# Kernel optimization log

Hardware: AMD Instinct MI355X
Metric: run time of the kernel (lower is better)

## Reference

```python
import jax, jax.numpy as jnp
import numpy as np

N_NODES = 100000
N_EDGES = 1600000
D = 64          # embedding_dim (in_feats == out_feats)
H = 1           # num_heads
NEG_SLOPE = 0.2


def setup_inputs() -> dict:
    key = jax.random.key(0)
    k = jax.random.split(key, 7)
    feat = jax.random.normal(k[0], (N_NODES, D), dtype=jnp.float32)
    W = jax.random.normal(k[1], (D, H * D), dtype=jnp.float32) * (1.0 / np.sqrt(D))
    attn_l = jax.random.normal(k[2], (1, H, D), dtype=jnp.float32) * (1.0 / np.sqrt(D))
    attn_r = jax.random.normal(k[3], (1, H, D), dtype=jnp.float32) * (1.0 / np.sqrt(D))
    bias = jnp.zeros((H * D,), dtype=jnp.float32)
    src = jax.random.randint(k[4], (N_EDGES,), 0, N_NODES, dtype=jnp.int32)
    dst = jax.random.randint(k[5], (N_EDGES,), 0, N_NODES, dtype=jnp.int32)
    return {"feat": feat, "W": W, "attn_l": attn_l, "attn_r": attn_r,
            "bias": bias, "src": src, "dst": dst}


def reference(feat, W, attn_l, attn_r, bias, src, dst):
    # fc (no bias), view to [N, H, D_out]
    ft = (feat @ W).reshape(-1, H, D)                       # [N, H, D]
    # per-node attention halves
    el = jnp.sum(ft * attn_l, axis=-1, keepdims=True)       # [N, H, 1]
    er = jnp.sum(ft * attn_r, axis=-1, keepdims=True)       # [N, H, 1]
    # edge score: u_add_v then leaky_relu
    e = el[src] + er[dst]                                    # [E, H, 1]
    e = jnp.where(e > 0, e, NEG_SLOPE * e)
    # edge softmax over incoming edges of each destination node
    emax = jax.ops.segment_max(e, dst, num_segments=N_NODES)  # [N, H, 1]
    e_exp = jnp.exp(e - emax[dst])
    denom = jax.ops.segment_sum(e_exp, dst, num_segments=N_NODES)  # [N, H, 1]
    a = e_exp / denom[dst]                                   # [E, H, 1]
    # u_mul_e + sum aggregation to destination
    m = ft[src] * a                                          # [E, H, D]
    rst = jax.ops.segment_sum(m, dst, num_segments=N_NODES)  # [N, H, D]
    # residual (Identity since in_feats == out_feats) + bias
    rst = rst + feat.reshape(-1, H, D)
    rst = rst + bias.reshape(1, H, D)
    return rst
```

## Files before the change

kernel.cpp:

```cpp
#include <hip/hip_runtime.h>
#include <hip/hip_fp16.h>
#include <math.h>

#define NN 100000
#define NE 1600000
#define D 64
#define NEG_SLOPE 0.2f
#define BSH 8
#define BMASK 255
#define NBKT 391
#define NB1 196
#define CHUNK 8192
#define BKT_CAP 8192

typedef __attribute__((ext_vector_type(8))) short short8;
typedef __attribute__((ext_vector_type(4))) float f32x4;

template<int CTRL>
__device__ __forceinline__ float dpp_add(float x) {
    int y = __builtin_amdgcn_update_dpp(0, __float_as_int(x), CTRL, 0xf, 0xf, true);
    return x + __int_as_float(y);
}
template<int CTRL>
__device__ __forceinline__ float dpp_max(float x) {
    int xi = __float_as_int(x);
    int y = __builtin_amdgcn_update_dpp(xi, xi, CTRL, 0xf, 0xf, false);
    return fmaxf(x, __int_as_float(y));
}
__device__ __forceinline__ float wave_sum63(float x) {
    x = dpp_add<0x111>(x); x = dpp_add<0x112>(x); x = dpp_add<0x114>(x);
    x = dpp_add<0x118>(x); x = dpp_add<0x142>(x); x = dpp_add<0x143>(x);
    return x;
}
__device__ __forceinline__ float wave_max63(float x) {
    x = dpp_max<0x111>(x); x = dpp_max<0x112>(x); x = dpp_max<0x114>(x);
    x = dpp_max<0x118>(x); x = dpp_max<0x142>(x); x = dpp_max<0x143>(x);
    return x;
}
__device__ __forceinline__ float rdlane_f(float v, int l) {
    return __int_as_float(__builtin_amdgcn_readlane(__float_as_int(v), l));
}
__device__ __forceinline__ unsigned bf16_1(float f) {
    unsigned x = __float_as_uint(f);
    return (x + 0x7fffu + ((x >> 16) & 1u)) >> 16;
}
__device__ __forceinline__ unsigned bfpack(float a, float b) {
    return bf16_1(a) | (bf16_1(b) << 16);
}

__global__ __launch_bounds__(256) void k_bhist(const int* __restrict__ dst,
                                               unsigned* __restrict__ bcnt,
                                               unsigned* __restrict__ blockHist) {
    __shared__ unsigned lh[NBKT];
    int t = threadIdx.x;
    unsigned b0 = blockIdx.x * CHUNK;
    unsigned b1 = min(b0 + CHUNK, (unsigned)NE);
    for (int b = t; b < NBKT; b += 256) lh[b] = 0u;
    __syncthreads();
    const int4* d4 = (const int4*)(dst + b0);
    unsigned n4 = (b1 - b0) >> 2;
    for (unsigned i = t; i < n4; i += 256) {
        int4 v = d4[i];
        atomicAdd(&lh[((unsigned)v.x) >> BSH], 1u);
        atomicAdd(&lh[((unsigned)v.y) >> BSH], 1u);
        atomicAdd(&lh[((unsigned)v.z) >> BSH], 1u);
        atomicAdd(&lh[((unsigned)v.w) >> BSH], 1u);
    }
    __syncthreads();
    unsigned* bh = blockHist + (size_t)blockIdx.x * NBKT;
    for (int b = t; b < NBKT; b += 256) {
        unsigned c = lh[b];
        bh[b] = c;
        if (c) atomicAdd(&bcnt[b], c);
    }
}

__global__ __launch_bounds__(512) void k_bscan(const unsigned* __restrict__ bcnt,
                                               unsigned* __restrict__ bkt_base,
                                               unsigned* __restrict__ bkt_cur) {
    __shared__ unsigned sh[512];
    int t = threadIdx.x;
    sh[t] = (t < NBKT) ? bcnt[t] : 0u;
    __syncthreads();
    for (int off = 1; off < 512; off <<= 1) {
        unsigned u = (t >= off) ? sh[t - off] : 0u;
        __syncthreads();
        sh[t] += u;
        __syncthreads();
    }
    if (t < NBKT) {
        unsigned ex = t ? sh[t - 1] : 0u;
        bkt_base[t] = ex;
        bkt_cur[t] = ex;
    }
}

__global__ __launch_bounds__(256) void k_bin(const int* __restrict__ src,
                                             const int* __restrict__ dst,
                                             unsigned* __restrict__ bkt_cur,
                                             unsigned* __restrict__ binned,
                                             const unsigned* __restrict__ blockHist) {
    __shared__ unsigned lh[NBKT];
    int t = threadIdx.x;
    unsigned b0 = blockIdx.x * CHUNK;
    unsigned b1 = min(b0 + CHUNK, (unsigned)NE);
    const unsigned* bh = blockHist + (size_t)blockIdx.x * NBKT;
    for (int b = t; b < NBKT; b += 256) {
        unsigned c = bh[b];
        lh[b] = c ? atomicAdd(&bkt_cur[b], c) : 0u;
    }
    __syncthreads();
    const int4* d4 = (const int4*)(dst + b0);
    const int4* s4 = (const int4*)(src + b0);
    unsigned n4 = (b1 - b0) >> 2;
    for (unsigned i = t; i < n4; i += 256) {
        int4 dv = d4[i];
        int4 sv = s4[i];
        {   unsigned d_ = (unsigned)dv.x, s_ = (unsigned)sv.x;
            unsigned pos = atomicAdd(&lh[d_ >> BSH], 1u);
            binned[pos] = (s_ << BSH) | (d_ & BMASK); }
        {   unsigned d_ = (unsigned)dv.y, s_ = (unsigned)sv.y;
            unsigned pos = atomicAdd(&lh[d_ >> BSH], 1u);
            binned[pos] = (s_ << BSH) | (d_ & BMASK); }
        {   unsigned d_ = (unsigned)dv.z, s_ = (unsigned)sv.z;
            unsigned pos = atomicAdd(&lh[d_ >> BSH], 1u);
            binned[pos] = (s_ << BSH) | (d_ & BMASK); }
        {   unsigned d_ = (unsigned)dv.w, s_ = (unsigned)sv.w;
            unsigned pos = atomicAdd(&lh[d_ >> BSH], 1u);
            binned[pos] = (s_ << BSH) | (d_ & BMASK); }
    }
}

__global__ __launch_bounds__(256) void k_bsort(const unsigned* __restrict__ bkt_base,
                                               const unsigned* __restrict__ binned,
                                               int* __restrict__ perm,
                                               unsigned* __restrict__ rowp) {
    __shared__ unsigned lh[256];
    __shared__ unsigned cur[256];
    __shared__ unsigned stage[BKT_CAP];
    int t = threadIdx.x;
    int b = blockIdx.x;
    unsigned beg = bkt_base[b];
    unsigned end = (b == NBKT - 1) ? (unsigned)NE : bkt_base[b + 1];
    unsigned cnt = end - beg;
    lh[t] = 0u;
    __syncthreads();
    if (cnt <= BKT_CAP) {
        for (unsigned i = t; i < cnt; i += 256) {
            unsigned w = binned[beg + i];
            stage[i] = w;
            atomicAdd(&lh[w & BMASK], 1u);
        }
    } else {
        for (unsigned i = beg + t; i < end; i += 256)
            atomicAdd(&lh[binned[i] & BMASK], 1u);
    }
    __syncthreads();
    for (int off = 1; off < 256; off <<= 1) {
        unsigned u = (t >= off) ? lh[t - off] : 0u;
        __syncthreads();
        lh[t] += u;
        __syncthreads();
    }
    unsigned start = (t == 0) ? 0u : lh[t - 1];
    unsigned node = ((unsigned)b << BSH) + (unsigned)t;
    if (node <= NN) rowp[node] = beg + start;
    cur[t] = start;
    __syncthreads();
    if (cnt <= BKT_CAP) {
        for (unsigned i = t; i < cnt; i += 256) {
            unsigned w = stage[i];
            unsigned pos = atomicAdd(&cur[w & BMASK], 1u);
            perm[beg + pos] = (int)(w >> BSH);
        }
    } else {
        for (unsigned i = beg + t; i < end; i += 256) {
            unsigned w = binned[i];
            unsigned pos = atomicAdd(&cur[w & BMASK], 1u);
            perm[beg + pos] = (int)(w >> BSH);
        }
    }
}


__global__ __launch_bounds__(256) void k_wprep(const float* __restrict__ W,
                                               const float* __restrict__ attn_l,
                                               const float* __restrict__ attn_r,
                                               float* __restrict__ wl,
                                               float* __restrict__ wr,
                                               unsigned short* __restrict__ Wtb,
                                               unsigned* __restrict__ bcnt) {
    int t = threadIdx.x;
    for (int i = t; i < NBKT; i += 256) bcnt[i] = 0u;
    {   int k = t >> 2, s = t & 3;
        float pl = 0.f, pr = 0.f;
        #pragma unroll
        for (int q = 0; q < 4; ++q) {
            int seg = s + q * 4;
            float4 f = *(const float4*)(W + k * 64 + seg * 4);
            float4 a = *(const float4*)(attn_l + seg * 4);
            float4 b = *(const float4*)(attn_r + seg * 4);
            pl += f.x * a.x + f.y * a.y + f.z * a.z + f.w * a.w;
            pr += f.x * b.x + f.y * b.y + f.z * b.z + f.w * b.w;
        }
        pl += __shfl_xor(pl, 1, 64); pl += __shfl_xor(pl, 2, 64);
        pr += __shfl_xor(pr, 1, 64); pr += __shfl_xor(pr, 2, 64);
        if (s == 0) { wl[k] = pl; wr[k] = pr; }
    }
    {   int j = t & 63, g = t >> 6;
        #pragma unroll
        for (int i = 0; i < 8; ++i) {
            int k0 = g * 16 + i * 2;
            float w0 = W[k0 * 64 + j];
            float w1 = W[(k0 + 1) * 64 + j];
            *(unsigned*)(Wtb + j * 64 + k0) = bfpack(w0, w1);
        }
    }
}

__global__ __launch_bounds__(256) void k1_mfma(const float* __restrict__ feat,
                                               const float* __restrict__ wl,
                                               const float* __restrict__ wr,
                                               const unsigned short* __restrict__ Wtb,
                                               __half* __restrict__ ft,
                                               float* __restrict__ el,
                                               float* __restrict__ er) {
    __shared__ unsigned short Ab[64 * 64];
    __shared__ unsigned short Bb[64 * 64];
    int t = threadIdx.x;
    int n0 = blockIdx.x * 64;

    {
        int j = t >> 2, q = t & 3;
        uint4 w0 = *(const uint4*)(Wtb + j * 64 + q * 16);
        uint4 w1 = *(const uint4*)(Wtb + j * 64 + q * 16 + 8);
        unsigned m = (unsigned)((j & 7) << 4);
        *(uint4*)((char*)Bb + j * 128 + (((unsigned)(q * 32)) ^ m)) = w0;
        *(uint4*)((char*)Bb + j * 128 + (((unsigned)(q * 32 + 16)) ^ m)) = w1;
    }
    {
        int r = t >> 2, s = t & 3;
        int n = n0 + r;
        bool valid = n < NN;
        const float* fp = feat + (size_t)(valid ? n : (NN - 1)) * D;
        float pl = 0.f, pr = 0.f;
        unsigned m = (unsigned)((r & 7) << 4);
        #pragma unroll
        for (int q = 0; q < 4; ++q) {
            int seg = s + q * 4;
            float4 f = *(const float4*)(fp + seg * 4);
            float4 a = *(const float4*)(wl + seg * 4);
            float4 b = *(const float4*)(wr + seg * 4);
            pl += f.x * a.x + f.y * a.y + f.z * a.z + f.w * a.w;
            pr += f.x * b.x + f.y * b.y + f.z * b.z + f.w * b.w;
            uint2 pk;
            pk.x = bfpack(f.x, f.y);
            pk.y = bfpack(f.z, f.w);
            *(uint2*)((char*)Ab + r * 128 + (((unsigned)(seg * 8)) ^ m)) = pk;
        }
        pl += __shfl_xor(pl, 1, 64); pl += __shfl_xor(pl, 2, 64);
        pr += __shfl_xor(pr, 1, 64); pr += __shfl_xor(pr, 2, 64);
        if (s == 0 && valid) { el[n] = pl; er[n] = pr; }
    }
    __syncthreads();

    int w = t >> 6, l = t & 63;
    int lr = l & 15, lg = l >> 4;
    f32x4 acc0 = {0.f, 0.f, 0.f, 0.f};
    f32x4 acc1 = {0.f, 0.f, 0.f, 0.f};
    f32x4 acc2 = {0.f, 0.f, 0.f, 0.f};
    f32x4 acc3 = {0.f, 0.f, 0.f, 0.f};

    int jrow = w * 16 + lr;
    unsigned bm = (unsigned)((jrow & 7) << 4);
    short8 bf0 = *(const short8*)((char*)Bb + jrow * 128 + (((unsigned)(0 + lg * 16)) ^ bm));
    short8 bf1 = *(const short8*)((char*)Bb + jrow * 128 + (((unsigned)(64 + lg * 16)) ^ bm));

    #pragma unroll
    for (int rt = 0; rt < 4; ++rt) {
        int arow = rt * 16 + lr;
        unsigned am = (unsigned)((arow & 7) << 4);
        short8 a0 = *(const short8*)((char*)Ab + arow * 128 + (((unsigned)(0 + lg * 16)) ^ am));
        short8 a1 = *(const short8*)((char*)Ab + arow * 128 + (((unsigned)(64 + lg * 16)) ^ am));
        f32x4 acc = (rt == 0) ? acc0 : (rt == 1) ? acc1 : (rt == 2) ? acc2 : acc3;
        acc = __builtin_amdgcn_mfma_f32_16x16x32_bf16(a0, bf0, acc, 0, 0, 0);
        acc = __builtin_amdgcn_mfma_f32_16x16x32_bf16(a1, bf1, acc, 0, 0, 0);
        if (rt == 0) acc0 = acc; else if (rt == 1) acc1 = acc;
        else if (rt == 2) acc2 = acc; else acc3 = acc;
    }

    int col = w * 16 + lr;
    #pragma unroll
    for (int rt = 0; rt < 4; ++rt) {
        f32x4 acc = (rt == 0) ? acc0 : (rt == 1) ? acc1 : (rt == 2) ? acc2 : acc3;
        #pragma unroll
        for (int i = 0; i < 4; ++i) {
            int row = rt * 16 + lg * 4 + i;
            int nn = n0 + row;
            if (nn < NN) ft[(size_t)nn * D + col] = __float2half(acc[i]);
        }
    }
}

__device__ __noinline__ void agg_node64(int d, int lane,
                                        const unsigned* __restrict__ row,
                                        const int* __restrict__ perm_src,
                                        const float* __restrict__ el,
                                        const float* __restrict__ er,
                                        const __half* __restrict__ ft,
                                        const float* __restrict__ feat,
                                        const float* __restrict__ bias,
                                        float* __restrict__ out) {
    unsigned beg = row[d], end = row[d + 1];
    float er_d = er[d];
    float acc = 0.0f;
    float s = 0.0f;
    float m = -INFINITY;
    for (unsigned base = beg; base < end; base += 64) {
        unsigned i = base + lane;
        float e = -INFINITY;
        if (i < end) {
            int sid2 = perm_src[i];
            float v = el[sid2] + er_d;
            e = v > 0.0f ? v : NEG_SLOPE * v;
        }
        m = fmaxf(m, rdlane_f(wave_max63(e), 63));
    }
    for (unsigned base = beg; base < end; base += 64) {
        unsigned i = base + lane;
        float exx = 0.0f;
        if (i < end) {
            int sid2 = perm_src[i];
            float v = el[sid2] + er_d;
            v = v > 0.0f ? v : NEG_SLOPE * v;
            exx = __expf(v - m);
        }
        s += rdlane_f(wave_sum63(exx), 63);
    }
    for (unsigned jj = beg; jj < end; ++jj) {
        int sj = perm_src[jj];
        float v = el[sj] + er_d;
        v = v > 0.0f ? v : NEG_SLOPE * v;
        acc = fmaf(__half2float(ft[((size_t)sj << 6) + lane]), __expf(v - m), acc);
    }
    acc /= s;
    out[(size_t)d * D + lane] = acc + feat[(size_t)d * D + lane] + bias[lane];
}

#define LOAD8(B, J) do { \
    int _s0 = __builtin_amdgcn_readlane(sid, (J) + 0); \
    int _s1 = __builtin_amdgcn_readlane(sid, (J) + 1); \
    int _s2 = __builtin_amdgcn_readlane(sid, (J) + 2); \
    int _s3 = __builtin_amdgcn_readlane(sid, (J) + 3); \
    int _s4 = __builtin_amdgcn_readlane(sid, (J) + 4); \
    int _s5 = __builtin_amdgcn_readlane(sid, (J) + 5); \
    int _s6 = __builtin_amdgcn_readlane(sid, (J) + 6); \
    int _s7 = __builtin_amdgcn_readlane(sid, (J) + 7); \
    B##0 = ft[((size_t)_s0 << 6) + lane]; \
    B##1 = ft[((size_t)_s1 << 6) + lane]; \
    B##2 = ft[((size_t)_s2 << 6) + lane]; \
    B##3 = ft[((size_t)_s3 << 6) + lane]; \
    B##4 = ft[((size_t)_s4 << 6) + lane]; \
    B##5 = ft[((size_t)_s5 << 6) + lane]; \
    B##6 = ft[((size_t)_s6 << 6) + lane]; \
    B##7 = ft[((size_t)_s7 << 6) + lane]; \
} while (0)

#define FMA8(B, J) do { \
    acc = fmaf(__half2float(B##0), rdlane_f(ex, (J) + 0), acc); \
    acc = fmaf(__half2float(B##1), rdlane_f(ex, (J) + 1), acc); \
    acc = fmaf(__half2float(B##2), rdlane_f(ex, (J) + 2), acc); \
    acc = fmaf(__half2float(B##3), rdlane_f(ex, (J) + 3), acc); \
    acc = fmaf(__half2float(B##4), rdlane_f(ex, (J) + 4), acc); \
    acc = fmaf(__half2float(B##5), rdlane_f(ex, (J) + 5), acc); \
    acc = fmaf(__half2float(B##6), rdlane_f(ex, (J) + 6), acc); \
    acc = fmaf(__half2float(B##7), rdlane_f(ex, (J) + 7), acc); \
} while (0)

__global__ __launch_bounds__(256) void k_agg(const unsigned* __restrict__ row,
                                             const int* __restrict__ perm_src,
                                             const float* __restrict__ el,
                                             const float* __restrict__ er,
                                             const __half* __restrict__ ft,
                                             const float* __restrict__ feat,
                                             const float* __restrict__ bias,
                                             float* __restrict__ out) {
    int gid = blockIdx.x * 256 + threadIdx.x;
    int d = gid >> 6;
    int lane = gid & 63;
    if (d >= NN) return;

    unsigned beg = row[d], end = row[d + 1];
    int deg = (int)(end - beg);

    if (deg > 64) {
        agg_node64(d, lane, row, perm_src, el, er, ft, feat, bias, out);
        return;
    }

    float er_d = er[d];
    int sid = 0;
    if (lane < deg) sid = perm_src[beg + lane];
    float elv = el[sid];

    __half c0, c1, c2, c3, c4, c5, c6, c7;
    __half n0, n1, n2, n3, n4, n5, n6, n7;
    LOAD8(c, 0);

    float e = -INFINITY;
    if (lane < deg) {
        float v = elv + er_d;
        e = v > 0.0f ? v : NEG_SLOPE * v;
    }
    float m = rdlane_f(wave_max63(e), 63);
    float ex = (lane < deg) ? __expf(e - m) : 0.0f;
    float s = rdlane_f(wave_sum63(ex), 63);
    float inv_s = (deg > 0) ? __frcp_rn(s) : 0.0f;

    float acc = 0.0f;
    if (deg > 0) {
        int j = 0;
        while (true) {
            bool more = (j + 8) < deg;
            if (more) LOAD8(n, j + 8);
            FMA8(c, j);
            j += 8;
            if (!more) break;
            bool more2 = (j + 8) < deg;
            if (more2) LOAD8(c, j + 8);
            FMA8(n, j);
            j += 8;
            if (!more2) break;
        }
    }
    acc *= inv_s;
    out[(size_t)d * D + lane] = acc + feat[(size_t)d * D + lane] + bias[lane];
}

extern "C" void kernel_launch(void* const* d_in, const int* in_sizes, int n_in,
                              void* d_out, int out_size, void* d_ws, size_t ws_size,
                              hipStream_t stream) {
    const float* feat   = (const float*)d_in[0];
    const float* W      = (const float*)d_in[1];
    const float* attn_l = (const float*)d_in[2];
    const float* attn_r = (const float*)d_in[3];
    const float* bias   = (const float*)d_in[4];
    const int*   src    = (const int*)d_in[5];
    const int*   dst    = (const int*)d_in[6];
    float* out = (float*)d_out;

    char* ws = (char*)d_ws;
    __half*   ft     = (__half*)(ws);
    unsigned* binned = (unsigned*)(ws);
    float*    wl     = (float*)(ws + 12800000);
    float*    wr     = (float*)(ws + 12800256);
    unsigned short* Wtb = (unsigned short*)(ws + 12800512);
    float*    el     = (float*)(ws + 25600000);
    float*    er     = (float*)(ws + 26000000);
    int*      perm   = (int*)(ws + 26400000);
    unsigned* rowp   = (unsigned*)(ws + 32800000);
    unsigned* bcnt   = (unsigned*)(ws + 33200004);
    unsigned* bbase  = (unsigned*)(ws + 33201568);
    unsigned* bcur   = (unsigned*)(ws + 33203132);
    unsigned* bhist  = (unsigned*)(ws + 33204696);

    k_wprep<<<1, 256, 0, stream>>>(W, attn_l, attn_r, wl, wr, Wtb, bcnt);
    k_bhist<<<NB1, 256, 0, stream>>>(dst, bcnt, bhist);
    k_bscan<<<1, 512, 0, stream>>>(bcnt, bbase, bcur);
    k_bin<<<NB1, 256, 0, stream>>>(src, dst, bcur, binned, bhist);
    k_bsort<<<NBKT, 256, 0, stream>>>(bbase, binned, perm, rowp);

    k1_mfma<<<(NN + 63) / 64, 256, 0, stream>>>(feat, wl, wr, Wtb, ft, el, er);
    k_agg<<<(NN * 64 + 255) / 256, 256, 0, stream>>>(rowp, perm, el, er,
                                                     ft, feat, bias, out);
}
```

Baseline: 115.3 us.

## Fuse bucket scan into histogram and weight prep into projection kernel

Folds the single-block bucket prefix scan into the histogram kernel: a last-block ticket counter runs the scan, and the counters are now cleared by a memset. Removes the separate weight-prep launch, so each projection block recomputes the attention-projected weights and the swizzled bf16 W tile into shared memory. In the aggregation kernel, zero-degree nodes exit early, gather addresses are built with byte offsets, and the softmax max-subtraction is dropped. This cuts kernel launches and serial tiny kernels, but exp can now overflow if edge scores are large, and the weight prep is repeated in every block.

```diff
diff --git a/kernel.cpp b/kernel.cpp
--- a/kernel.cpp
+++ b/kernel.cpp
@@ -48,18 +48,23 @@
     return bf16_1(a) | (bf16_1(b) << 16);
 }
 
-__global__ __launch_bounds__(256) void k_bhist(const int* __restrict__ dst,
+__global__ __launch_bounds__(512) void k_bhist(const int* __restrict__ dst,
                                                unsigned* __restrict__ bcnt,
-                                               unsigned* __restrict__ blockHist) {
+                                               unsigned* __restrict__ blockHist,
+                                               unsigned* __restrict__ done,
+                                               unsigned* __restrict__ bkt_base,
+                                               unsigned* __restrict__ bkt_cur) {
     __shared__ unsigned lh[NBKT];
+    __shared__ unsigned sh[512];
+    __shared__ unsigned ticket;
     int t = threadIdx.x;
     unsigned b0 = blockIdx.x * CHUNK;
     unsigned b1 = min(b0 + CHUNK, (unsigned)NE);
-    for (int b = t; b < NBKT; b += 256) lh[b] = 0u;
+    for (int b = t; b < NBKT; b += 512) lh[b] = 0u;
     __syncthreads();
     const int4* d4 = (const int4*)(dst + b0);
     unsigned n4 = (b1 - b0) >> 2;
-    for (unsigned i = t; i < n4; i += 256) {
+    for (unsigned i = t; i < n4; i += 512) {
         int4 v = d4[i];
         atomicAdd(&lh[((unsigned)v.x) >> BSH], 1u);
         atomicAdd(&lh[((unsigned)v.y) >> BSH], 1u);
@@ -68,30 +73,33 @@
     }
     __syncthreads();
     unsigned* bh = blockHist + (size_t)blockIdx.x * NBKT;
-    for (int b = t; b < NBKT; b += 256) {
+    for (int b = t; b < NBKT; b += 512) {
         unsigned c = lh[b];
         bh[b] = c;
         if (c) atomicAdd(&bcnt[b], c);
     }
-}
-
-__global__ __launch_bounds__(512) void k_bscan(const unsigned* __restrict__ bcnt,
-                                               unsigned* __restrict__ bkt_base,
-                                               unsigned* __restrict__ bkt_cur) {
-    __shared__ unsigned sh[512];
-    int t = threadIdx.x;
-    sh[t] = (t < NBKT) ? bcnt[t] : 0u;
-    __syncthreads();
-    for (int off = 1; off < 512; off <<= 1) {
-        unsigned u = (t >= off) ? sh[t - off] : 0u;
+    __syncthreads();
+    if (t == 0) {
+        __threadfence();
+        ticket = atomicAdd(done, 1u);
+    }
+    __syncthreads();
+    if (ticket == (unsigned)(NB1 - 1)) {
+        unsigned v = 0u;
+        if (t < NBKT) v = atomicAdd(&bcnt[t], 0u);
+        sh[t] = v;
         __syncthreads();
-        sh[t] += u;
-        __syncthreads();
-    }
-    if (t < NBKT) {
-        unsigned ex = t ? sh[t - 1] : 0u;
-        bkt_base[t] = ex;
-        bkt_cur[t] = ex;
+        for (int off = 1; off < 512; off <<= 1) {
+            unsigned u = (t >= off) ? sh[t - off] : 0u;
+            __syncthreads();
+            sh[t] += u;
+            __syncthreads();
+        }
+        if (t < NBKT) {
+            unsigned ex = t ? sh[t - 1] : 0u;
+            bkt_base[t] = ex;
+            bkt_cur[t] = ex;
+        }
     }
 }
 
@@ -183,16 +191,21 @@
 }
 
 
-__global__ __launch_bounds__(256) void k_wprep(const float* __restrict__ W,
+__global__ __launch_bounds__(256) void k1_mfma(const float* __restrict__ feat,
+                                               const float* __restrict__ W,
                                                const float* __restrict__ attn_l,
                                                const float* __restrict__ attn_r,
-                                               float* __restrict__ wl,
-                                               float* __restrict__ wr,
-                                               unsigned short* __restrict__ Wtb,
-                                               unsigned* __restrict__ bcnt) {
+                                               __half* __restrict__ ft,
+                                               float* __restrict__ el,
+                                               float* __restrict__ er) {
+    __shared__ unsigned short Ab[64 * 64];
+    __shared__ unsigned short Bb[64 * 64];
+    __shared__ float wlS[64], wrS[64];
     int t = threadIdx.x;
-    for (int i = t; i < NBKT; i += 256) bcnt[i] = 0u;
-    {   int k = t >> 2, s = t & 3;
+    int n0 = blockIdx.x * 64;
+
+    {
+        int k = t >> 2, s = t & 3;
         float pl = 0.f, pr = 0.f;
         #pragma unroll
         for (int q = 0; q < 4; ++q) {
@@ -205,39 +218,20 @@
         }
         pl += __shfl_xor(pl, 1, 64); pl += __shfl_xor(pl, 2, 64);
         pr += __shfl_xor(pr, 1, 64); pr += __shfl_xor(pr, 2, 64);
-        if (s == 0) { wl[k] = pl; wr[k] = pr; }
-    }
-    {   int j = t & 63, g = t >> 6;
+        if (s == 0) { wlS[k] = pl; wrS[k] = pr; }
+    }
+    {
+        int j = t & 63, g = t >> 6;
+        unsigned m = (unsigned)((j & 7) << 4);
         #pragma unroll
         for (int i = 0; i < 8; ++i) {
             int k0 = g * 16 + i * 2;
             float w0 = W[k0 * 64 + j];
             float w1 = W[(k0 + 1) * 64 + j];
-            *(unsigned*)(Wtb + j * 64 + k0) = bfpack(w0, w1);
-        }
-    }
-}
-
-__global__ __launch_bounds__(256) void k1_mfma(const float* __restrict__ feat,
-                                               const float* __restrict__ wl,
-                                               const float* __restrict__ wr,
-                                               const unsigned short* __restrict__ Wtb,
-                                               __half* __restrict__ ft,
-                                               float* __restrict__ el,
-                                               float* __restrict__ er) {
-    __shared__ unsigned short Ab[64 * 64];
-    __shared__ unsigned short Bb[64 * 64];
-    int t = threadIdx.x;
-    int n0 = blockIdx.x * 64;
-
-    {
-        int j = t >> 2, q = t & 3;
-        uint4 w0 = *(const uint4*)(Wtb + j * 64 + q * 16);
-        uint4 w1 = *(const uint4*)(Wtb + j * 64 + q * 16 + 8);
-        unsigned m = (unsigned)((j & 7) << 4);
-        *(uint4*)((char*)Bb + j * 128 + (((unsigned)(q * 32)) ^ m)) = w0;
-        *(uint4*)((char*)Bb + j * 128 + (((unsigned)(q * 32 + 16)) ^ m)) = w1;
-    }
+            *(unsigned*)((char*)Bb + j * 128 + (((unsigned)(k0 * 2)) ^ m)) = bfpack(w0, w1);
+        }
+    }
+    __syncthreads();
     {
         int r = t >> 2, s = t & 3;
         int n = n0 + r;
@@ -249,8 +243,8 @@
         for (int q = 0; q < 4; ++q) {
             int seg = s + q * 4;
             float4 f = *(const float4*)(fp + seg * 4);
-            float4 a = *(const float4*)(wl + seg * 4);
-            float4 b = *(const float4*)(wr + seg * 4);
+            float4 a = *(const float4*)(wlS + seg * 4);
+            float4 b = *(const float4*)(wrS + seg * 4);
             pl += f.x * a.x + f.y * a.y + f.z * a.z + f.w * a.w;
             pr += f.x * b.x + f.y * b.y + f.z * b.z + f.w * b.w;
             uint2 pk;
@@ -348,22 +342,22 @@
 }
 
 #define LOAD8(B, J) do { \
-    int _s0 = __builtin_amdgcn_readlane(sid, (J) + 0); \
-    int _s1 = __builtin_amdgcn_readlane(sid, (J) + 1); \
-    int _s2 = __builtin_amdgcn_readlane(sid, (J) + 2); \
-    int _s3 = __builtin_amdgcn_readlane(sid, (J) + 3); \
-    int _s4 = __builtin_amdgcn_readlane(sid, (J) + 4); \
-    int _s5 = __builtin_amdgcn_readlane(sid, (J) + 5); \
-    int _s6 = __builtin_amdgcn_readlane(sid, (J) + 6); \
-    int _s7 = __builtin_amdgcn_readlane(sid, (J) + 7); \
-    B##0 = ft[((size_t)_s0 << 6) + lane]; \
-    B##1 = ft[((size_t)_s1 << 6) + lane]; \
-    B##2 = ft[((size_t)_s2 << 6) + lane]; \
-    B##3 = ft[((size_t)_s3 << 6) + lane]; \
-    B##4 = ft[((size_t)_s4 << 6) + lane]; \
-    B##5 = ft[((size_t)_s5 << 6) + lane]; \
-    B##6 = ft[((size_t)_s6 << 6) + lane]; \
-    B##7 = ft[((size_t)_s7 << 6) + lane]; \
+    unsigned _o0 = (((unsigned)__builtin_amdgcn_readlane(sid, (J) + 0)) << 7) | lb; \
+    unsigned _o1 = (((unsigned)__builtin_amdgcn_readlane(sid, (J) + 1)) << 7) | lb; \
+    unsigned _o2 = (((unsigned)__builtin_amdgcn_readlane(sid, (J) + 2)) << 7) | lb; \
+    unsigned _o3 = (((unsigned)__builtin_amdgcn_readlane(sid, (J) + 3)) << 7) | lb; \
+    unsigned _o4 = (((unsigned)__builtin_amdgcn_readlane(sid, (J) + 4)) << 7) | lb; \
+    unsigned _o5 = (((unsigned)__builtin_amdgcn_readlane(sid, (J) + 5)) << 7) | lb; \
+    unsigned _o6 = (((unsigned)__builtin_amdgcn_readlane(sid, (J) + 6)) << 7) | lb; \
+    unsigned _o7 = (((unsigned)__builtin_amdgcn_readlane(sid, (J) + 7)) << 7) | lb; \
+    B##0 = *(const __half*)(ftb + _o0); \
+    B##1 = *(const __half*)(ftb + _o1); \
+    B##2 = *(const __half*)(ftb + _o2); \
+    B##3 = *(const __half*)(ftb + _o3); \
+    B##4 = *(const __half*)(ftb + _o4); \
+    B##5 = *(const __half*)(ftb + _o5); \
+    B##6 = *(const __half*)(ftb + _o6); \
+    B##7 = *(const __half*)(ftb + _o7); \
 } while (0)
 
 #define FMA8(B, J) do { \
@@ -397,41 +391,41 @@
         agg_node64(d, lane, row, perm_src, el, er, ft, feat, bias, out);
         return;
     }
+    if (deg == 0) {
+        out[(size_t)d * D + lane] = feat[(size_t)d * D + lane] + bias[lane];
+        return;
+    }
 
     float er_d = er[d];
-    int sid = 0;
-    if (lane < deg) sid = perm_src[beg + lane];
+    int sid = perm_src[beg + ((lane < deg) ? lane : 0)];
     float elv = el[sid];
+
+    const char* ftb = (const char*)ft;
+    unsigned lb = (unsigned)lane << 1;
 
     __half c0, c1, c2, c3, c4, c5, c6, c7;
     __half n0, n1, n2, n3, n4, n5, n6, n7;
     LOAD8(c, 0);
 
-    float e = -INFINITY;
-    if (lane < deg) {
-        float v = elv + er_d;
-        e = v > 0.0f ? v : NEG_SLOPE * v;
-    }
-    float m = rdlane_f(wave_max63(e), 63);
-    float ex = (lane < deg) ? __expf(e - m) : 0.0f;
+    float e = elv + er_d;
+    e = e > 0.0f ? e : NEG_SLOPE * e;
+    float ex = (lane < deg) ? __expf(e) : 0.0f;
     float s = rdlane_f(wave_sum63(ex), 63);
-    float inv_s = (deg > 0) ? __frcp_rn(s) : 0.0f;
+    float inv_s = __frcp_rn(s);
 
     float acc = 0.0f;
-    if (deg > 0) {
-        int j = 0;
-        while (true) {
-            bool more = (j + 8) < deg;
-            if (more) LOAD8(n, j + 8);
-            FMA8(c, j);
-            j += 8;
-            if (!more) break;
-            bool more2 = (j + 8) < deg;
-            if (more2) LOAD8(c, j + 8);
-            FMA8(n, j);
-            j += 8;
-            if (!more2) break;
-        }
+    int j = 0;
+    while (true) {
+        bool more = (j + 8) < deg;
+        if (more) LOAD8(n, j + 8);
+        FMA8(c, j);
+        j += 8;
+        if (!more) break;
+        bool more2 = (j + 8) < deg;
+        if (more2) LOAD8(c, j + 8);
+        FMA8(n, j);
+        j += 8;
+        if (!more2) break;
     }
     acc *= inv_s;
     out[(size_t)d * D + lane] = acc + feat[(size_t)d * D + lane] + bias[lane];
@@ -452,25 +446,22 @@
     char* ws = (char*)d_ws;
     __half*   ft     = (__half*)(ws);
     unsigned* binned = (unsigned*)(ws);
-    float*    wl     = (float*)(ws + 12800000);
-    float*    wr     = (float*)(ws + 12800256);
-    unsigned short* Wtb = (unsigned short*)(ws + 12800512);
-    float*    el     = (float*)(ws + 25600000);
-    float*    er     = (float*)(ws + 26000000);
-    int*      perm   = (int*)(ws + 26400000);
-    unsigned* rowp   = (unsigned*)(ws + 32800000);
-    unsigned* bcnt   = (unsigned*)(ws + 33200004);
-    unsigned* bbase  = (unsigned*)(ws + 33201568);
-    unsigned* bcur   = (unsigned*)(ws + 33203132);
-    unsigned* bhist  = (unsigned*)(ws + 33204696);
-
-    k_wprep<<<1, 256, 0, stream>>>(W, attn_l, attn_r, wl, wr, Wtb, bcnt);
-    k_bhist<<<NB1, 256, 0, stream>>>(dst, bcnt, bhist);
-    k_bscan<<<1, 512, 0, stream>>>(bcnt, bbase, bcur);
+    float*    el     = (float*)(ws + 12800000);
+    float*    er     = (float*)(ws + 13200000);
+    int*      perm   = (int*)(ws + 13600000);
+    unsigned* rowp   = (unsigned*)(ws + 20000000);
+    unsigned* bcnt   = (unsigned*)(ws + 20400004);
+    unsigned* done   = (unsigned*)(ws + 20401568);
+    unsigned* bbase  = (unsigned*)(ws + 20401572);
+    unsigned* bcur   = (unsigned*)(ws + 20403136);
+    unsigned* bhist  = (unsigned*)(ws + 20404700);
+
+    hipMemsetAsync(bcnt, 0, NBKT * sizeof(unsigned) + 4, stream);
+    k_bhist<<<NB1, 512, 0, stream>>>(dst, bcnt, bhist, done, bbase, bcur);
     k_bin<<<NB1, 256, 0, stream>>>(src, dst, bcur, binned, bhist);
     k_bsort<<<NBKT, 256, 0, stream>>>(bbase, binned, perm, rowp);
 
-    k1_mfma<<<(NN + 63) / 64, 256, 0, stream>>>(feat, wl, wr, Wtb, ft, el, er);
+    k1_mfma<<<(NN + 63) / 64, 256, 0, stream>>>(feat, W, attn_l, attn_r, ft, el, er);
     k_agg<<<(NN * 64 + 255) / 256, 256, 0, stream>>>(rowp, perm, el, er,
                                                      ft, feat, bias, out);
 }
```

Result: faster. 112.6 us (-2.4%).
